# Kernel optimization log

Hardware: AMD Instinct MI355X
Metric: run time of the kernel (lower is better)

## Reference

```python
import jax, jax.numpy as jnp
from jax import lax
import numpy as np

D_MODEL = 1024
D_STATE = 16
D_CONV = 4
EXPAND = 2
D_INNER = EXPAND * D_MODEL  # 2048
DT_RANK = D_MODEL // 16     # 64
BATCH = 2
SEQLEN = 1024


def setup_inputs() -> dict:
    key = jax.random.key(0)
    ks = iter(jax.random.split(key, 32))

    def nrm(shape, s=0.02):
        return jax.random.normal(next(ks), shape, jnp.float32) * s

    def mamba_params():
        return dict(
            Win=nrm((2 * D_INNER, D_MODEL)), bin=jnp.zeros((2 * D_INNER,), jnp.float32),
            convw=nrm((D_INNER, D_CONV), 0.1), convb=jnp.zeros((D_INNER,), jnp.float32),
            Wx=nrm((DT_RANK + 2 * D_STATE, D_INNER)),
            Wdt=nrm((D_INNER, DT_RANK), 0.1), bdt=nrm((D_INNER,), 0.1),
            Alog=jnp.log(jnp.broadcast_to(jnp.arange(1, D_STATE + 1, dtype=jnp.float32), (D_INNER, D_STATE))),
            Dsk=jnp.ones((D_INNER,), jnp.float32),
            Wout=nrm((D_MODEL, D_INNER)), bout=jnp.zeros((D_MODEL,), jnp.float32),
        )

    inp = {"x": jax.random.normal(next(ks), (BATCH, SEQLEN, D_MODEL), jnp.float32)}
    for pref, p in (("f_", mamba_params()), ("b_", mamba_params())):
        for k, v in p.items():
            inp[pref + k] = v
    inp["proj_W"] = nrm((D_MODEL, 2 * D_MODEL))
    inp["proj_b"] = jnp.zeros((D_MODEL,), jnp.float32)
    return inp


def selective_scan(u, delta, A, Bm, Cm, Dsk):
    # u, delta: (B,L,Di); Bm, Cm: (B,L,N); A: (Di,N); Dsk: (Di,)
    def step(h, inp):
        u_t, d_t, b_t, c_t = inp  # (B,Di),(B,Di),(B,N),(B,N)
        dA = jnp.exp(d_t[..., None] * A)                      # (B,Di,N)
        h = h * dA + (d_t * u_t)[..., None] * b_t[:, None, :]  # (B,Di,N)
        y = jnp.einsum('bdn,bn->bd', h, c_t)
        return h, y

    h0 = jnp.zeros((u.shape[0], A.shape[0], A.shape[1]), u.dtype)
    xs = (u.transpose(1, 0, 2), delta.transpose(1, 0, 2),
          Bm.transpose(1, 0, 2), Cm.transpose(1, 0, 2))
    _, ys = lax.scan(step, h0, xs)
    return ys.transpose(1, 0, 2) + u * Dsk  # (B,L,Di)


def mamba_fwd(x, Win, bin_, convw, convb, Wx, Wdt, bdt, Alog, Dsk, Wout, bout):
    xz = x @ Win.T + bin_                      # (B,L,2*Di)
    xin, z = jnp.split(xz, 2, axis=-1)
    # causal depthwise conv over time: (B,Di,L)
    xc = lax.conv_general_dilated(
        xin.transpose(0, 2, 1), convw[:, None, :], (1,), [(D_CONV - 1, 0)],
        dimension_numbers=('NCH', 'OIH', 'NCH'), feature_group_count=D_INNER)
    u = jax.nn.silu(xc.transpose(0, 2, 1) + convb)  # (B,L,Di)
    xdbl = u @ Wx.T                                 # (B,L,dt_rank+2N)
    dt, Bm, Cm = jnp.split(xdbl, [DT_RANK, DT_RANK + D_STATE], axis=-1)
    delta = jax.nn.softplus(dt @ Wdt.T + bdt)       # (B,L,Di)
    A = -jnp.exp(Alog)
    y = selective_scan(u, delta, A, Bm, Cm, Dsk)
    y = y * jax.nn.silu(z)
    return y @ Wout.T + bout


def reference(x,
              f_Win, f_bin, f_convw, f_convb, f_Wx, f_Wdt, f_bdt, f_Alog, f_Dsk, f_Wout, f_bout,
              b_Win, b_bin, b_convw, b_convb, b_Wx, b_Wdt, b_bdt, b_Alog, b_Dsk, b_Wout, b_bout,
              proj_W, proj_b):
    out_f = mamba_fwd(x, f_Win, f_bin, f_convw, f_convb, f_Wx, f_Wdt, f_bdt, f_Alog, f_Dsk, f_Wout, f_bout)
    xr = jnp.flip(x, axis=1)
    out_b = mamba_fwd(xr, b_Win, b_bin, b_convw, b_convb, b_Wx, b_Wdt, b_bdt, b_Alog, b_Dsk, b_Wout, b_bout)
    out_b = jnp.flip(out_b, axis=1)
    out = jnp.concatenate([out_f, out_b], axis=-1)  # (B,L,2*d_model)
    return out @ proj_W.T + proj_b
```

## Files before the change

### kernel.cpp

```cpp
#include <hip/hip_runtime.h>
#include <math.h>

#define D_MODEL 1024
#define D_STATE 16
#define D_CONV  4
#define D_INNER 2048
#define DT_RANK 64
#define BATCH   2
#define SEQLEN  1024
#define MROWS   2048
#define XDBL_LD 128
#define NCHUNK  32
#define CLEN    (SEQLEN / NCHUNK)
#define NCHG    8192

typedef __attribute__((ext_vector_type(8))) short bf16x8;
typedef __attribute__((ext_vector_type(4))) float f32x4;

#define BARR() asm volatile("s_barrier" ::: "memory")
#define VMW(n) asm volatile("s_waitcnt vmcnt(" #n ")" ::: "memory")
#define LGKM(n) asm volatile("s_waitcnt lgkmcnt(" #n ")" ::: "memory")
#define SCHB() __builtin_amdgcn_sched_barrier(0)

static __device__ __forceinline__ float sigmoidf_(float x) {
    return 1.f / (1.f + __expf(-x));
}
static __device__ __forceinline__ unsigned short bf16rn(float f) {
    unsigned u = __float_as_uint(f);
    return (unsigned short)((u + 0x7FFFu + ((u >> 16) & 1u)) >> 16);
}
static __device__ __forceinline__ void hl_split(float f, unsigned short& h, unsigned short& l) {
    h = bf16rn(f);
    l = bf16rn(f - __uint_as_float((unsigned)h << 16));
}
static __device__ __forceinline__ float us2f(unsigned short u) {
    return __uint_as_float((unsigned)u << 16);
}

static __device__ __forceinline__
void split_block(const float* __restrict__ in, int R, int C, int ldin,
                 unsigned short* __restrict__ out, int Rout, bool flip,
                 int blk, int tid)
{
    int q = blk * 256 + tid;
    int qpr = C >> 2;
    int row = q / qpr;
    int c4 = (q - row * qpr) << 2;
    if (row >= Rout) return;
    unsigned short h[4] = {0, 0, 0, 0}, l[4] = {0, 0, 0, 0};
    if (row < R) {
        int sr = row;
        if (flip) { int b = row >> 10, t = row & 1023; sr = (b << 10) + (1023 - t); }
        float4 v = *(const float4*)(in + (size_t)sr * ldin + c4);
        float f[4] = {v.x, v.y, v.z, v.w};
        #pragma unroll
        for (int i = 0; i < 4; ++i) hl_split(f[i], h[i], l[i]);
    }
    size_t ob = (size_t)row * (2 * C);
    *(ushort4*)(out + ob + c4)     = make_ushort4(h[0], h[1], h[2], h[3]);
    *(ushort4*)(out + ob + C + c4) = make_ushort4(l[0], l[1], l[2], l[3]);
}

__global__ __launch_bounds__(256)
void prep1_kernel(const float* __restrict__ x,
                  const float* __restrict__ Win0, const float* __restrict__ Win1,
                  const float* __restrict__ Wx0,  const float* __restrict__ Wx1,
                  const float* __restrict__ Wdt0, const float* __restrict__ Wdt1,
                  unsigned short* xc0,
                  unsigned short* Winb0, unsigned short* Winb1,
                  unsigned short* Wxb0, unsigned short* Wxb1,
                  unsigned short* Wdtb0, unsigned short* Wdtb1)
{
    int b = blockIdx.x, tid = threadIdx.x;
    if      (b < 2048)  split_block(x,    MROWS, D_MODEL, D_MODEL, xc0,  MROWS, false, b,        tid);
    else if (b < 6144)  split_block(Win0, 4096,  D_MODEL, D_MODEL, Winb0, 4096, false, b - 2048, tid);
    else if (b < 10240) split_block(Win1, 4096,  D_MODEL, D_MODEL, Winb1, 4096, false, b - 6144, tid);
    else if (b < 10496) split_block(Wx0,  96,    D_INNER, D_INNER, Wxb0,  128,  false, b - 10240, tid);
    else if (b < 10752) split_block(Wx1,  96,    D_INNER, D_INNER, Wxb1,  128,  false, b - 10496, tid);
    else if (b < 10880) split_block(Wdt0, D_INNER, DT_RANK, DT_RANK, Wdtb0, D_INNER, false, b - 10752, tid);
    else                split_block(Wdt1, D_INNER, DT_RANK, DT_RANK, Wdtb1, D_INNER, false, b - 10880, tid);
}

#define SWZ(row) (((row) >> 1) & 3)
#define RDA(p, kk, row) (*(const bf16x8*)&AS[p][kk][row][(fs ^ SWZ(row)) << 3])
#define RDB(p, kk, row) (*(const bf16x8*)&BS[p][kk][row][(fs ^ SWZ(row)) << 3])

#define MFMA16(ACCBASE, AF, BF) \
    _Pragma("unroll") for (int f = 0; f < 4; ++f) \
    _Pragma("unroll") for (int g = 0; g < 4; ++g) \
        acc[(ACCBASE) + f][g] = __builtin_amdgcn_mfma_f32_16x16x32_bf16(AF[f], BF[g], acc[(ACCBASE) + f][g], 0, 0, 0);

#define KTILE(MODE, kt) do { \
    const int p_ = (kt) & 1; \
    const int pn_ = ((kt) + 1) & 1; \
    {  \
        if (MODE < 2) stageA((kt) + 1, 1); \
        BARR(); \
        _Pragma("unroll") for (int f = 0; f < 4; ++f) { int rw = wm + 64 + f * 16 + fr; aFB[f] = RDA(p_, 0, rw); } \
        LGKM(4); SCHB(); \
        __builtin_amdgcn_s_setprio(1); \
        MFMA16(0, aFA, bFA) \
        __builtin_amdgcn_s_setprio(0); \
    } \
    {  \
        if (MODE == 0) stageB((kt) + 2, 0); \
        BARR(); \
        _Pragma("unroll") for (int f = 0; f < 4; ++f) { int rw = wm + f * 16 + fr; aFA[f] = RDA(p_, 1, rw); } \
        _Pragma("unroll") for (int g = 0; g < 4; ++g) { int rw = wn + g * 16 + fr; bFB[g] = RDB(p_, 1, rw); } \
        LGKM(8); SCHB(); \
        __builtin_amdgcn_s_setprio(1); \
        MFMA16(4, aFB, bFA) \
        __builtin_amdgcn_s_setprio(0); \
    } \
    {  \
        if (MODE == 0) stageA((kt) + 2, 0); \
        BARR(); \
        _Pragma("unroll") for (int f = 0; f < 4; ++f) { int rw = wm + 64 + f * 16 + fr; aFB[f] = RDA(p_, 1, rw); } \
        LGKM(4); SCHB(); \
        __builtin_amdgcn_s_setprio(1); \
        MFMA16(0, aFA, bFB) \
        __builtin_amdgcn_s_setprio(0); \
    } \
    {  \
        if (MODE == 0) { VMW(4); } else if (MODE == 1) { VMW(0); } \
        if (MODE == 0) stageB((kt) + 2, 1); \
        BARR(); \
        if (MODE < 2) { \
            _Pragma("unroll") for (int f = 0; f < 4; ++f) { int rw = wm + f * 16 + fr; aFA[f] = RDA(pn_, 0, rw); } \
            _Pragma("unroll") for (int g = 0; g < 4; ++g) { int rw = wn + g * 16 + fr; bFA[g] = RDB(pn_, 0, rw); } \
            LGKM(8); \
        } else { LGKM(0); } \
        SCHB(); \
        __builtin_amdgcn_s_setprio(1); \
        MFMA16(4, aFB, bFB) \
        __builtin_amdgcn_s_setprio(0); \
    } \
} while (0)

template<int ACT, bool PART, int KTS, bool DUALN>
__global__ __launch_bounds__(512, 1)
void gemm256(const unsigned short* __restrict__ A0,
             const unsigned short* __restrict__ A1,
             const unsigned short* __restrict__ W0,
             const unsigned short* __restrict__ W1,
             const float* __restrict__ bias0,
             const float* __restrict__ bias1,
             float* __restrict__ C0, float* __restrict__ C1,
             float* __restrict__ part,
             int ldc, int N, int K, int nks)
{
    __shared__ unsigned short AS[2][2][256][32];
    __shared__ unsigned short BS[2][2][256][32];

    const int tid = threadIdx.x;
    const int lane = tid & 63;
    const int wid = tid >> 6;

    const int z = blockIdx.z;
    const int zdir = z / nks;
    const int ks = z - zdir * nks;

    const int nbx = gridDim.x;
    const int nwg = nbx * gridDim.y;
    int bid = blockIdx.y * nbx + blockIdx.x;
    int q8 = nwg >> 3;
    int swz = (bid & 7) * q8 + (bid >> 3);
    const int bm = (swz / nbx) * 256;
    const int bn = (swz % nbx) * 256;

    int dn, bnn;
    if (DUALN) { dn = (bn >= (N >> 1)) ? 1 : 0; bnn = bn - dn * (N >> 1); }
    else       { dn = zdir; bnn = bn; }
    const unsigned short* A = (DUALN || dn == 0) ? A0 : A1;
    const unsigned short* W = dn ? W1 : W0;

    const int ldg = 2 * K;
    constexpr int NT = 3 * KTS;
    const int Kc = KTS * 64;
    const int kbase = ks * Kc;

    const int wm = (wid >> 2) * 128;
    const int wn = (wid & 3) * 64;
    const int fr = lane & 15;
    const int fs = lane >> 4;

    f32x4 acc[8][4];
    #pragma unroll
    for (int i = 0; i < 8; ++i)
        #pragma unroll
        for (int j = 0; j < 4; ++j) {
            f32x4 zv = {0.f, 0.f, 0.f, 0.f};
            acc[i][j] = zv;
        }

    auto koffA = [&](int t) { unsigned tu = (unsigned)t; unsigned sg = tu / KTS;
                              unsigned w = tu - sg * KTS;
                              return (int)((sg == 1 ? (unsigned)K : 0u) + kbase + w * 64); };
    auto koffB = [&](int t) { unsigned tu = (unsigned)t; unsigned sg = tu / KTS;
                              unsigned w = tu - sg * KTS;
                              return (int)((sg == 2 ? (unsigned)K : 0u) + kbase + w * 64); };

    auto stageA = [&](int t, int kk) {
        int ko = koffA(t) + kk * 32;
        unsigned short* dst = &AS[t & 1][kk][0][0];
        #pragma unroll
        for (int i = 0; i < 2; ++i) {
            int s = i * 512 + tid;
            int row = s >> 2, sl = s & 3, lsl = sl ^ SWZ(row);
            const unsigned short* src = A + (size_t)(bm + row) * ldg + ko + lsl * 8;
            __builtin_amdgcn_global_load_lds(
                (const __attribute__((address_space(1))) void*)src,
                (__attribute__((address_space(3))) void*)(dst + s * 8), 16, 0, 0);
        }
    };
    auto stageB = [&](int t, int kk) {
        int ko = koffB(t) + kk * 32;
        unsigned short* dst = &BS[t & 1][kk][0][0];
        #pragma unroll
        for (int i = 0; i < 2; ++i) {
            int s = i * 512 + tid;
            int row = s >> 2, sl = s & 3, lsl = sl ^ SWZ(row);
            const unsigned short* src = W + (size_t)(bnn + row) * ldg + ko + lsl * 8;
            __builtin_amdgcn_global_load_lds(
                (const __attribute__((address_space(1))) void*)src,
                (__attribute__((address_space(3))) void*)(dst + s * 8), 16, 0, 0);
        }
    };

    stageB(0, 0); stageA(0, 0); stageB(0, 1); stageA(0, 1);
    stageB(1, 0); stageA(1, 0); stageB(1, 1);
    VMW(6);
    BARR();

    bf16x8 aFA[4], aFB[4], bFA[4], bFB[4];
    #pragma unroll
    for (int f = 0; f < 4; ++f) { int rw = wm + f * 16 + fr; aFA[f] = RDA(0, 0, rw); }
    #pragma unroll
    for (int g = 0; g < 4; ++g) { int rw = wn + g * 16 + fr; bFA[g] = RDB(0, 0, rw); }

    #pragma unroll 1
    for (int kt = 0; kt < NT - 2; ++kt) KTILE(0, kt);
    KTILE(1, NT - 2);
    KTILE(2, NT - 1);

    if (PART) {
        float* P = part + (size_t)z * ((size_t)MROWS * N);
        #pragma unroll
        for (int i = 0; i < 8; ++i)
            #pragma unroll
            for (int j = 0; j < 4; ++j) {
                int coln = bnn + wn + j * 16 + fr;
                #pragma unroll
                for (int r = 0; r < 4; ++r) {
                    int rowm = bm + wm + i * 16 + fs * 4 + r;
                    P[(size_t)rowm * N + coln] = acc[i][j][r];
                }
            }
    } else {
        const float* bias = dn ? bias1 : bias0;
        float* C = dn ? C1 : C0;
        #pragma unroll
        for (int i = 0; i < 8; ++i)
            #pragma unroll
            for (int j = 0; j < 4; ++j) {
                int coln = bnn + wn + j * 16 + fr;
                float bv = bias ? bias[coln] : 0.f;
                #pragma unroll
                for (int r = 0; r < 4; ++r) {
                    int rowm = bm + wm + i * 16 + fs * 4 + r;
                    float v = acc[i][j][r] + bv;
                    if (ACT == 1) v = (v > 20.f) ? v : log1pf(__expf(v));
                    int crow = rowm;
                    if (DUALN && dn) { int bb = rowm >> 10, t = rowm & 1023; crow = (bb << 10) + 1023 - t; }
                    C[(size_t)crow * ldc + coln] = v;
                }
            }
    }
}

template<int ACT, bool PART>
__global__ __launch_bounds__(256)
void gemm_mfma(const unsigned short* __restrict__ A0,
               const unsigned short* __restrict__ A1,
               const unsigned short* __restrict__ W0,
               const unsigned short* __restrict__ W1,
               const float* __restrict__ bias0,
               const float* __restrict__ bias1,
               float* __restrict__ C0, float* __restrict__ C1,
               float* __restrict__ part,
               int ldc, int N, int K, int nks)
{
    __shared__ __align__(16) unsigned short As[128 * 32];
    __shared__ __align__(16) unsigned short Bs[128 * 32];

    const int tid = threadIdx.x;
    const int lane = tid & 63;
    const int wid = tid >> 6;

    const int z = blockIdx.z;
    const int dir = z / nks;
    const int ks = z - dir * nks;
    const unsigned short* A = dir ? A1 : A0;
    const unsigned short* W = dir ? W1 : W0;

    const int nbx = gridDim.x;
    const int nwg = nbx * gridDim.y;
    int bid = blockIdx.y * nbx + blockIdx.x;
    int q8 = nwg >> 3;
    int swz = (nwg >= 8) ? (bid & 7) * q8 + (bid >> 3) : bid;
    const int bm = (swz / nbx) * 128;
    const int bn = (swz % nbx) * 128;

    const int ldg = 2 * K;
    const int Kc = K / nks;
    const int kbase = ks * Kc;

    f32x4 acc[4][4];
    #pragma unroll
    for (int i = 0; i < 4; ++i)
        #pragma unroll
        for (int j = 0; j < 4; ++j) {
            f32x4 zv = {0.f, 0.f, 0.f, 0.f};
            acc[i][j] = zv;
        }

    const int r0 = tid >> 2;
    const int k0s = (tid & 3) ^ ((r0 >> 1) & 3);
    const int r1 = (256 + tid) >> 2;
    const int k1s = (tid & 3) ^ ((r1 >> 1) & 3);

    unsigned short* As_w0 = &As[(tid >> 2) * 32 + ((tid & 3) << 3)];
    unsigned short* As_w1 = As_w0 + 64 * 32;
    unsigned short* Bs_w0 = &Bs[(tid >> 2) * 32 + ((tid & 3) << 3)];
    unsigned short* Bs_w1 = Bs_w0 + 64 * 32;

    const int wm = (wid >> 1) * 64;
    const int wn = (wid & 1) * 64;
    const int fr = lane & 15;
    const int fs = lane >> 4;

    const int KS = Kc >> 5;
    #pragma unroll 1
    for (int seg = 0; seg < 3; ++seg) {
        const int aoff = ((seg == 1) ? K : 0) + kbase;
        const int boff = ((seg == 2) ? K : 0) + kbase;
        #pragma unroll 1
        for (int kt = 0; kt < KS; ++kt) {
            const int kk = kt << 5;
            const unsigned short* ga0 = A + (size_t)(bm + r0) * ldg + aoff + kk + k0s * 8;
            const unsigned short* ga1 = A + (size_t)(bm + r1) * ldg + aoff + kk + k1s * 8;
            const unsigned short* gw0 = W + (size_t)(bn + r0) * ldg + boff + kk + k0s * 8;
            const unsigned short* gw1 = W + (size_t)(bn + r1) * ldg + boff + kk + k1s * 8;
            __builtin_amdgcn_global_load_lds(
                (const __attribute__((address_space(1))) void*)ga0,
                (__attribute__((address_space(3))) void*)As_w0, 16, 0, 0);
            __builtin_amdgcn_global_load_lds(
                (const __attribute__((address_space(1))) void*)ga1,
                (__attribute__((address_space(3))) void*)As_w1, 16, 0, 0);
            __builtin_amdgcn_global_load_lds(
                (const __attribute__((address_space(1))) void*)gw0,
                (__attribute__((address_space(3))) void*)Bs_w0, 16, 0, 0);
            __builtin_amdgcn_global_load_lds(
                (const __attribute__((address_space(1))) void*)gw1,
                (__attribute__((address_space(3))) void*)Bs_w1, 16, 0, 0);
            __syncthreads();

            bf16x8 aF[4], bF[4];
            #pragma unroll
            for (int f = 0; f < 4; ++f) {
                int ra = wm + f * 16 + fr;
                int sa = fs ^ ((ra >> 1) & 3);
                aF[f] = *(const bf16x8*)&As[ra * 32 + sa * 8];
                int rb = wn + f * 16 + fr;
                int sb = fs ^ ((rb >> 1) & 3);
                bF[f] = *(const bf16x8*)&Bs[rb * 32 + sb * 8];
            }
            #pragma unroll
            for (int i = 0; i < 4; ++i)
                #pragma unroll
                for (int j = 0; j < 4; ++j)
                    acc[i][j] = __builtin_amdgcn_mfma_f32_16x16x32_bf16(
                        aF[i], bF[j], acc[i][j], 0, 0, 0);
            __syncthreads();
        }
    }

    if (PART) {
        float* P = part + (size_t)z * ((size_t)MROWS * N);
        #pragma unroll
        for (int i = 0; i < 4; ++i)
            #pragma unroll
            for (int j = 0; j < 4; ++j) {
                int coln = bn + wn + j * 16 + fr;
                #pragma unroll
                for (int r = 0; r < 4; ++r) {
                    int rowm = bm + wm + i * 16 + fs * 4 + r;
                    P[(size_t)rowm * N + coln] = acc[i][j][r];
                }
            }
    } else {
        const float* bias = dir ? bias1 : bias0;
        float* C = dir ? C1 : C0;
        #pragma unroll
        for (int i = 0; i < 4; ++i)
            #pragma unroll
            for (int j = 0; j < 4; ++j) {
                int coln = bn + wn + j * 16 + fr;
                float bv = bias ? bias[coln] : 0.f;
                #pragma unroll
                for (int r = 0; r < 4; ++r) {
                    int rowm = bm + wm + i * 16 + fs * 4 + r;
                    float v = acc[i][j][r] + bv;
                    if (ACT == 1) v = (v > 20.f) ? v : log1pf(__expf(v));
                    C[(size_t)rowm * ldc + coln] = v;
                }
            }
    }
}

__global__ __launch_bounds__(256)
void reduce_xdbl_k(const float* __restrict__ part,
                   float* __restrict__ xdbl0, float* __restrict__ xdbl1,
                   unsigned short* __restrict__ dtb0, unsigned short* __restrict__ dtb1)
{
    const int dz = blockIdx.z;
    const float* P = part + (size_t)dz * 16 * MROWS * XDBL_LD;
    float* xdbl = dz ? xdbl1 : xdbl0;
    unsigned short* dtb = dz ? dtb1 : dtb0;
    int i = blockIdx.x * 256 + threadIdx.x;
    int row = i >> 5;
    int c4 = (i & 31) << 2;
    float4 s = make_float4(0.f, 0.f, 0.f, 0.f);
    #pragma unroll
    for (int k = 0; k < 16; ++k) {
        float4 v = *(const float4*)(P + (size_t)k * MROWS * XDBL_LD + (size_t)row * XDBL_LD + c4);
        s.x += v.x; s.y += v.y; s.z += v.z; s.w += v.w;
    }
    *(float4*)(xdbl + (size_t)row * XDBL_LD + c4) = s;
    if (c4 < DT_RANK) {
        float f[4] = {s.x, s.y, s.z, s.w};
        unsigned short h[4], l[4];
        #pragma unroll
        for (int j = 0; j < 4; ++j) hl_split(f[j], h[j], l[j]);
        *(ushort4*)(dtb + (size_t)row * (2 * DT_RANK) + c4) = make_ushort4(h[0], h[1], h[2], h[3]);
        *(ushort4*)(dtb + (size_t)row * (2 * DT_RANK) + DT_RANK + c4) = make_ushort4(l[0], l[1], l[2], l[3]);
    }
}

__global__ __launch_bounds__(256)
void mid_kernel(const float* __restrict__ part2,
                const float* __restrict__ bout0, const float* __restrict__ bout1,
                unsigned short* __restrict__ tmpb,
                const float* __restrict__ projW, unsigned short* __restrict__ pWb)
{
    const int dz = blockIdx.z;
    const int tid = threadIdx.x;
    if (dz == 2) {
        split_block(projW, D_MODEL, 2 * D_MODEL, 2 * D_MODEL, pWb, D_MODEL, false, blockIdx.x, tid);
        return;
    }
    const float* P = part2 + (size_t)dz * 4 * MROWS * D_MODEL;
    const float* bias = dz ? bout1 : bout0;
    const int colofs = dz ? D_MODEL : 0;
    int i = blockIdx.x * 256 + tid;
    int row = i >> 8;
    int c4 = (i & 255) << 2;
    float4 s = make_float4(bias[c4], bias[c4 + 1], bias[c4 + 2], bias[c4 + 3]);
    #pragma unroll
    for (int k = 0; k < 4; ++k) {
        float4 v = *(const float4*)(P + (size_t)k * MROWS * D_MODEL + (size_t)row * D_MODEL + c4);
        s.x += v.x; s.y += v.y; s.z += v.z; s.w += v.w;
    }
    int orow = row;
    if (dz) { int bb = row >> 10, t = row & 1023; orow = (bb << 10) + 1023 - t; }
    float f[4] = {s.x, s.y, s.z, s.w};
    unsigned short h[4], l[4];
    #pragma unroll
    for (int j = 0; j < 4; ++j) hl_split(f[j], h[j], l[j]);
    *(ushort4*)(tmpb + (size_t)orow * 4096 + colofs + c4) = make_ushort4(h[0], h[1], h[2], h[3]);
    *(ushort4*)(tmpb + (size_t)orow * 4096 + 2048 + colofs + c4) = make_ushort4(l[0], l[1], l[2], l[3]);
}

__global__ __launch_bounds__(256)
void reduce_out_k(const float* __restrict__ part, const float* __restrict__ bias,
                  float* __restrict__ out)
{
    int i = blockIdx.x * 256 + threadIdx.x;
    int row = i >> 8;
    int c4 = (i & 255) << 2;
    float4 s = make_float4(bias[c4], bias[c4 + 1], bias[c4 + 2], bias[c4 + 3]);
    #pragma unroll
    for (int k = 0; k < 8; ++k) {
        float4 v = *(const float4*)(part + (size_t)k * MROWS * D_MODEL + (size_t)row * D_MODEL + c4);
        s.x += v.x; s.y += v.y; s.z += v.z; s.w += v.w;
    }
    *(float4*)(out + (size_t)row * D_MODEL + c4) = s;
}

__global__ __launch_bounds__(256)
void conv_prep_kernel(const float* __restrict__ xz0, const float* __restrict__ xz1,
                      const float* __restrict__ cw0, const float* __restrict__ cw1,
                      const float* __restrict__ cb0, const float* __restrict__ cb1,
                      unsigned short* __restrict__ ub0, unsigned short* __restrict__ ub1,
                      const float* __restrict__ Wout0, const float* __restrict__ Wout1,
                      unsigned short* __restrict__ Woutb0, unsigned short* __restrict__ Woutb1)
{
    const int dz = blockIdx.z;
    const int tid = threadIdx.x;
    if (dz == 2) {
        int b = blockIdx.x;
        if (b < 2048) split_block(Wout0, D_MODEL, D_INNER, D_INNER, Woutb0, D_MODEL, false, b, tid);
        else if (b < 4096) split_block(Wout1, D_MODEL, D_INNER, D_INNER, Woutb1, D_MODEL, false, b - 2048, tid);
        return;
    }
    const float* xz = dz ? xz1 : xz0;
    const float* convw = dz ? cw1 : cw0;
    const float* convb = dz ? cb1 : cb0;
    unsigned short* ub = dz ? ub1 : ub0;
    int idx = blockIdx.x * 256 + tid;
    int d = idx % D_INNER;
    int r = idx / D_INNER;
    int t = r % SEQLEN;
    float acc = convb[d];
    #pragma unroll
    for (int k = 0; k < D_CONV; ++k) {
        int back = D_CONV - 1 - k;
        if (t - back >= 0)
            acc += xz[(size_t)(r - back) * (2 * D_INNER) + d] * convw[d * D_CONV + k];
    }
    float v = acc * sigmoidf_(acc);
    unsigned short h, l;
    hl_split(v, h, l);
    ub[(size_t)r * (2 * D_INNER) + d] = h;
    ub[(size_t)r * (2 * D_INNER) + D_INNER + d] = l;
}

__global__ __launch_bounds__(256)
void scan_phase1(const float* __restrict__ delta0, const float* __restrict__ delta1,
                 const unsigned short* __restrict__ ub0, const unsigned short* __restrict__ ub1,
                 const float* __restrict__ xdbl0, const float* __restrict__ xdbl1,
                 const float* __restrict__ Alog0, const float* __restrict__ Alog1,
                 float* __restrict__ aprod, float* __restrict__ hfin)
{
    const int gid = blockIdx.x * 256 + threadIdx.x;
    const int chg = gid & (NCHG - 1);
    const int chunk = gid >> 13;
    const int dir = chg >> 12;
    const int bd = chg & 4095;
    const int b = bd >> 11, d = bd & 2047;
    const float* delta = dir ? delta1 : delta0;
    const unsigned short* ub = dir ? ub1 : ub0;
    const float* xdbl = dir ? xdbl1 : xdbl0;
    const float* Alog = dir ? Alog1 : Alog0;

    float Av[16], h[16], ap[16];
    #pragma unroll
    for (int n = 0; n < 16; ++n) {
        Av[n] = -__expf(Alog[d * D_STATE + n]);
        h[n] = 0.f; ap[n] = 1.f;
    }
    const int t0 = chunk * CLEN;
    for (int t = t0; t < t0 + CLEN; ++t) {
        const size_t r = (size_t)b * SEQLEN + t;
        float dlt = delta[r * D_INNER + d];
        float uu = us2f(ub[r * 4096 + d]) + us2f(ub[r * 4096 + 2048 + d]);
        float du = dlt * uu;
        float4 bq[4];
        #pragma unroll
        for (int q = 0; q < 4; ++q)
            bq[q] = *(const float4*)(xdbl + r * XDBL_LD + DT_RANK + q * 4);
        #pragma unroll
        for (int n = 0; n < 16; ++n) {
            float Bv = ((const float*)&bq[n >> 2])[n & 3];
            float dA = __expf(dlt * Av[n]);
            h[n] = h[n] * dA + du * Bv;
            ap[n] *= dA;
        }
    }
    float* pa = aprod + (size_t)chunk * (NCHG * 16) + (size_t)chg * 16;
    float* pf = hfin  + (size_t)chunk * (NCHG * 16) + (size_t)chg * 16;
    #pragma unroll
    for (int q = 0; q < 4; ++q) {
        *(float4*)(pa + q * 4) = make_float4(ap[q*4], ap[q*4+1], ap[q*4+2], ap[q*4+3]);
        *(float4*)(pf + q * 4) = make_float4(h[q*4], h[q*4+1], h[q*4+2], h[q*4+3]);
    }
}

__global__ __launch_bounds__(256)
void scan_phase2(float* __restrict__ aprod ,
                 const float* __restrict__ hfin)
{
    const int gid = blockIdx.x * 256 + threadIdx.x;
    float h = 0.f;
    for (int c = 0; c < NCHUNK; ++c) {
        const size_t idx = (size_t)c * (NCHG * 16) + gid;
        float a = aprod[idx];
        float f = hfin[idx];
        aprod[idx] = h;
        h = a * h + f;
    }
}

__global__ __launch_bounds__(256)
void scan_phase3(const float* __restrict__ delta0, const float* __restrict__ delta1,
                 unsigned short* __restrict__ ub0, unsigned short* __restrict__ ub1,
                 const float* __restrict__ xdbl0, const float* __restrict__ xdbl1,
                 const float* __restrict__ Alog0, const float* __restrict__ Alog1,
                 const float* __restrict__ Dsk0, const float* __restrict__ Dsk1,
                 const float* __restrict__ xz0, const float* __restrict__ xz1,
                 const float* __restrict__ hin)
{
    const int gid = blockIdx.x * 256 + threadIdx.x;
    const int chg = gid & (NCHG - 1);
    const int chunk = gid >> 13;
    const int dir = chg >> 12;
    const int bd = chg & 4095;
    const int b = bd >> 11, d = bd & 2047;
    const float* delta = dir ? delta1 : delta0;
    unsigned short* ub = dir ? ub1 : ub0;
    const float* xdbl = dir ? xdbl1 : xdbl0;
    const float* Alog = dir ? Alog1 : Alog0;
    const float* Dsk = dir ? Dsk1 : Dsk0;
    const float* xz = dir ? xz1 : xz0;

    float Av[16], h[16];
    const float* ph = hin + (size_t)chunk * (NCHG * 16) + (size_t)chg * 16;
    #pragma unroll
    for (int n = 0; n < 16; ++n) {
        Av[n] = -__expf(Alog[d * D_STATE + n]);
        h[n] = ph[n];
    }
    const float Dv = Dsk[d];
    const int t0 = chunk * CLEN;
    for (int t = t0; t < t0 + CLEN; ++t) {
        const size_t r = (size_t)b * SEQLEN + t;
        float dlt = delta[r * D_INNER + d];
        float uu = us2f(ub[r * 4096 + d]) + us2f(ub[r * 4096 + 2048 + d]);
        float du = dlt * uu;
        float4 bq[4], cq[4];
        #pragma unroll
        for (int q = 0; q < 4; ++q) {
            bq[q] = *(const float4*)(xdbl + r * XDBL_LD + DT_RANK + q * 4);
            cq[q] = *(const float4*)(xdbl + r * XDBL_LD + DT_RANK + D_STATE + q * 4);
        }
        float p0 = 0.f, p1 = 0.f, p2 = 0.f, p3 = 0.f;
        #pragma unroll
        for (int n = 0; n < 16; ++n) {
            float Bv = ((const float*)&bq[n >> 2])[n & 3];
            float Cv = ((const float*)&cq[n >> 2])[n & 3];
            float dA = __expf(dlt * Av[n]);
            h[n] = h[n] * dA + du * Bv;
            if ((n & 3) == 0) p0 += h[n] * Cv;
            else if ((n & 3) == 1) p1 += h[n] * Cv;
            else if ((n & 3) == 2) p2 += h[n] * Cv;
            else p3 += h[n] * Cv;
        }
        float y = ((p0 + p1) + (p2 + p3)) + uu * Dv;
        float zv = xz[r * (2 * D_INNER) + D_INNER + d];
        float v = y * (zv * sigmoidf_(zv));
        unsigned short hh, ll;
        hl_split(v, hh, ll);
        ub[r * 4096 + d] = hh;
        ub[r * 4096 + 2048 + d] = ll;
    }
}

extern "C" void kernel_launch(void* const* d_in, const int* in_sizes, int n_in,
                              void* d_out, int out_size, void* d_ws, size_t ws_size,
                              hipStream_t stream)
{
    const float* x = (const float*)d_in[0];
    const float* proj_W = (const float*)d_in[23];
    const float* proj_b = (const float*)d_in[24];
    float* out = (float*)d_out;

    const float *Win[2], *bin_[2], *convw[2], *convb[2], *Wx[2], *Wdt[2], *bdt[2],
                *Alog[2], *Dsk[2], *Wout[2], *bout[2];
    for (int dir = 0; dir < 2; ++dir) {
        const int base = 1 + dir * 11;
        Win[dir]   = (const float*)d_in[base + 0];
        bin_[dir]  = (const float*)d_in[base + 1];
        convw[dir] = (const float*)d_in[base + 2];
        convb[dir] = (const float*)d_in[base + 3];
        Wx[dir]    = (const float*)d_in[base + 4];
        Wdt[dir]   = (const float*)d_in[base + 5];
        bdt[dir]   = (const float*)d_in[base + 6];
        Alog[dir]  = (const float*)d_in[base + 7];
        Dsk[dir]   = (const float*)d_in[base + 8];
        Wout[dir]  = (const float*)d_in[base + 9];
        bout[dir]  = (const float*)d_in[base + 10];
    }

    char* ws = (char*)d_ws;
    const size_t MB = 1ull << 20;
    float* xz[2]            = {(float*)(ws + 0 * MB),   (float*)(ws + 32 * MB)};
    unsigned short* ub[2]   = {(unsigned short*)(ws + 64 * MB),
                               (unsigned short*)(ws + 80 * MB)};
    unsigned short* Winb[2] = {(unsigned short*)(ws + 96 * MB),
                               (unsigned short*)(ws + 112 * MB)};
    unsigned short* xc0     = (unsigned short*)(ws + 128 * MB);
    float* part             = (float*)(ws + 112 * MB);
    float* part2            = (float*)(ws + 0 * MB);
    float* delta[2]         = {(float*)(ws + 112 * MB), (float*)(ws + 128 * MB)};
    unsigned short* Woutb[2]= {(unsigned short*)(ws + 96 * MB),
                               (unsigned short*)(ws + 104 * MB)};
    unsigned short* yzb[2]  = {ub[0], ub[1]};
    unsigned short* tmpb    = ub[0];
    unsigned short* pWb     = ub[1];
    unsigned short* Wxb[2]  = {(unsigned short*)(ws + 144 * MB), (unsigned short*)(ws + 145 * MB)};
    unsigned short* Wdtb[2] = {(unsigned short*)(ws + 146 * MB), (unsigned short*)(ws + 146 * MB + 512 * 1024)};
    unsigned short* dtb[2]  = {(unsigned short*)(ws + 147 * MB), (unsigned short*)(ws + 147 * MB + 512 * 1024)};
    float* xdbl[2]          = {(float*)(ws + 148 * MB), (float*)(ws + 149 * MB)};
    float* aprod            = (float*)(ws + 150 * MB);
    float* hfin             = (float*)(ws + 167 * MB);

    dim3 blk(256);

    prep1_kernel<<<11008, blk, 0, stream>>>(
        x, Win[0], Win[1], Wx[0], Wx[1], Wdt[0], Wdt[1],
        xc0, Winb[0], Winb[1], Wxb[0], Wxb[1], Wdtb[0], Wdtb[1]);

    gemm256<0, false, 16, true><<<dim3(32, 8, 1), dim3(512), 0, stream>>>(
        xc0, nullptr, Winb[0], Winb[1], bin_[0], bin_[1], xz[0], xz[1],
        nullptr, 4096, 8192, D_MODEL, 1);

    conv_prep_kernel<<<dim3((MROWS * D_INNER) / 256, 1, 3), blk, 0, stream>>>(
        xz[0], xz[1], convw[0], convw[1], convb[0], convb[1], ub[0], ub[1],
        Wout[0], Wout[1], Woutb[0], Woutb[1]);

    gemm_mfma<0, true><<<dim3(1, 16, 32), blk, 0, stream>>>(
        ub[0], ub[1], Wxb[0], Wxb[1], nullptr, nullptr, nullptr, nullptr,
        part, XDBL_LD, XDBL_LD, D_INNER, 16);

    reduce_xdbl_k<<<dim3(256, 1, 2), blk, 0, stream>>>(
        part, xdbl[0], xdbl[1], dtb[0], dtb[1]);

    gemm_mfma<1, false><<<dim3(16, 16, 2), blk, 0, stream>>>(
        dtb[0], dtb[1], Wdtb[0], Wdtb[1], bdt[0], bdt[1], delta[0], delta[1],
        nullptr, D_INNER, D_INNER, DT_RANK, 1);

    scan_phase1<<<NCHUNK * NCHG / 256, blk, 0, stream>>>(
        delta[0], delta[1], ub[0], ub[1], xdbl[0], xdbl[1], Alog[0], Alog[1],
        aprod, hfin);
    scan_phase2<<<NCHG * 16 / 256, blk, 0, stream>>>(aprod, hfin);
    scan_phase3<<<NCHUNK * NCHG / 256, blk, 0, stream>>>(
        delta[0], delta[1], ub[0], ub[1], xdbl[0], xdbl[1], Alog[0], Alog[1],
        Dsk[0], Dsk[1], xz[0], xz[1], aprod);

    gemm256<0, true, 8, false><<<dim3(4, 8, 8), dim3(512), 0, stream>>>(
        yzb[0], yzb[1], Woutb[0], Woutb[1], nullptr, nullptr, nullptr, nullptr,
        part2, D_MODEL, D_MODEL, D_INNER, 4);

    mid_kernel<<<dim3(2048, 1, 3), blk, 0, stream>>>(
        part2, bout[0], bout[1], tmpb, proj_W, pWb);

    gemm256<0, true, 4, false><<<dim3(4, 8, 8), dim3(512), 0, stream>>>(
        tmpb, nullptr, pWb, nullptr, nullptr, nullptr, nullptr, nullptr,
        part2, D_MODEL, D_MODEL, 2 * D_MODEL, 8);

    reduce_out_k<<<2048, blk, 0, stream>>>(part2, proj_b, out);
}
```

Baseline: 459.0 us.

## Replace 256x256 GEMM tiles with 128x128 tiles and halve split-K partitions

The 512-thread 256x256-tile GEMM is replaced by a 256-thread 128x128-tile kernel with two blocks per CU, a simpler double-buffered k-loop and half the accumulators. Split-K factors for the output and projection GEMMs are halved, and the reduction kernels are updated to match, which cuts partial-sum traffic. More and smaller blocks should improve occupancy and load balance across CUs. The cost is less data reuse per tile, so more global and LDS traffic is needed per FLOP.

```diff
diff --git a/kernel.cpp b/kernel.cpp
--- a/kernel.cpp
+++ b/kernel.cpp
@@ -85,72 +85,53 @@
 #define RDA(p, kk, row) (*(const bf16x8*)&AS[p][kk][row][(fs ^ SWZ(row)) << 3])
 #define RDB(p, kk, row) (*(const bf16x8*)&BS[p][kk][row][(fs ^ SWZ(row)) << 3])
 
-#define MFMA16(ACCBASE, AF, BF) \
+#define MFMA16(AF, BF) \
     _Pragma("unroll") for (int f = 0; f < 4; ++f) \
     _Pragma("unroll") for (int g = 0; g < 4; ++g) \
-        acc[(ACCBASE) + f][g] = __builtin_amdgcn_mfma_f32_16x16x32_bf16(AF[f], BF[g], acc[(ACCBASE) + f][g], 0, 0, 0);
-
-#define KTILE(MODE, kt) do { \
+        acc[f][g] = __builtin_amdgcn_mfma_f32_16x16x32_bf16(AF[f], BF[g], acc[f][g], 0, 0, 0);
+
+#define KT128(MODE, kt) do { \
     const int p_ = (kt) & 1; \
     const int pn_ = ((kt) + 1) & 1; \
     {  \
-        if (MODE < 2) stageA((kt) + 1, 1); \
+        if (MODE == 0) { stageA((kt) + 1, 0); stageB((kt) + 1, 0); VMW(4); } \
+        else { VMW(0); } \
         BARR(); \
-        _Pragma("unroll") for (int f = 0; f < 4; ++f) { int rw = wm + 64 + f * 16 + fr; aFB[f] = RDA(p_, 0, rw); } \
-        LGKM(4); SCHB(); \
+        _Pragma("unroll") for (int f = 0; f < 4; ++f) { int rw = wm + f * 16 + fr; aFB[f] = RDA(p_, 1, rw); } \
+        _Pragma("unroll") for (int g = 0; g < 4; ++g) { int rw = wn + g * 16 + fr; bFB[g] = RDB(p_, 1, rw); } \
+        LGKM(8); SCHB(); \
         __builtin_amdgcn_s_setprio(1); \
-        MFMA16(0, aFA, bFA) \
+        MFMA16(aFA, bFA) \
         __builtin_amdgcn_s_setprio(0); \
     } \
     {  \
-        if (MODE == 0) stageB((kt) + 2, 0); \
-        BARR(); \
-        _Pragma("unroll") for (int f = 0; f < 4; ++f) { int rw = wm + f * 16 + fr; aFA[f] = RDA(p_, 1, rw); } \
-        _Pragma("unroll") for (int g = 0; g < 4; ++g) { int rw = wn + g * 16 + fr; bFB[g] = RDB(p_, 1, rw); } \
-        LGKM(8); SCHB(); \
-        __builtin_amdgcn_s_setprio(1); \
-        MFMA16(4, aFB, bFA) \
-        __builtin_amdgcn_s_setprio(0); \
-    } \
-    {  \
-        if (MODE == 0) stageA((kt) + 2, 0); \
-        BARR(); \
-        _Pragma("unroll") for (int f = 0; f < 4; ++f) { int rw = wm + 64 + f * 16 + fr; aFB[f] = RDA(p_, 1, rw); } \
-        LGKM(4); SCHB(); \
-        __builtin_amdgcn_s_setprio(1); \
-        MFMA16(0, aFA, bFB) \
-        __builtin_amdgcn_s_setprio(0); \
-    } \
-    {  \
-        if (MODE == 0) { VMW(4); } else if (MODE == 1) { VMW(0); } \
-        if (MODE == 0) stageB((kt) + 2, 1); \
-        BARR(); \
-        if (MODE < 2) { \
+        if (MODE == 0) { \
+            stageA((kt) + 1, 1); stageB((kt) + 1, 1); VMW(4); BARR(); \
             _Pragma("unroll") for (int f = 0; f < 4; ++f) { int rw = wm + f * 16 + fr; aFA[f] = RDA(pn_, 0, rw); } \
             _Pragma("unroll") for (int g = 0; g < 4; ++g) { int rw = wn + g * 16 + fr; bFA[g] = RDB(pn_, 0, rw); } \
             LGKM(8); \
         } else { LGKM(0); } \
         SCHB(); \
         __builtin_amdgcn_s_setprio(1); \
-        MFMA16(4, aFB, bFB) \
+        MFMA16(aFB, bFB) \
         __builtin_amdgcn_s_setprio(0); \
     } \
 } while (0)
 
 template<int ACT, bool PART, int KTS, bool DUALN>
-__global__ __launch_bounds__(512, 1)
-void gemm256(const unsigned short* __restrict__ A0,
-             const unsigned short* __restrict__ A1,
-             const unsigned short* __restrict__ W0,
-             const unsigned short* __restrict__ W1,
-             const float* __restrict__ bias0,
-             const float* __restrict__ bias1,
-             float* __restrict__ C0, float* __restrict__ C1,
-             float* __restrict__ part,
-             int ldc, int N, int K, int nks)
-{
-    __shared__ unsigned short AS[2][2][256][32];
-    __shared__ unsigned short BS[2][2][256][32];
+__global__ __launch_bounds__(256, 2)
+void gemm128p(const unsigned short* __restrict__ A0,
+              const unsigned short* __restrict__ A1,
+              const unsigned short* __restrict__ W0,
+              const unsigned short* __restrict__ W1,
+              const float* __restrict__ bias0,
+              const float* __restrict__ bias1,
+              float* __restrict__ C0, float* __restrict__ C1,
+              float* __restrict__ part,
+              int ldc, int N, int K, int nks)
+{
+    __shared__ unsigned short AS[2][2][128][32];
+    __shared__ unsigned short BS[2][2][128][32];
 
     const int tid = threadIdx.x;
     const int lane = tid & 63;
@@ -165,8 +146,8 @@
     int bid = blockIdx.y * nbx + blockIdx.x;
     int q8 = nwg >> 3;
     int swz = (bid & 7) * q8 + (bid >> 3);
-    const int bm = (swz / nbx) * 256;
-    const int bn = (swz % nbx) * 256;
+    const int bm = (swz / nbx) * 128;
+    const int bn = (swz % nbx) * 128;
 
     int dn, bnn;
     if (DUALN) { dn = (bn >= (N >> 1)) ? 1 : 0; bnn = bn - dn * (N >> 1); }
@@ -179,14 +160,14 @@
     const int Kc = KTS * 64;
     const int kbase = ks * Kc;
 
-    const int wm = (wid >> 2) * 128;
-    const int wn = (wid & 3) * 64;
+    const int wm = (wid >> 1) * 64;
+    const int wn = (wid & 1) * 64;
     const int fr = lane & 15;
     const int fs = lane >> 4;
 
-    f32x4 acc[8][4];
-    #pragma unroll
-    for (int i = 0; i < 8; ++i)
+    f32x4 acc[4][4];
+    #pragma unroll
+    for (int i = 0; i < 4; ++i)
         #pragma unroll
         for (int j = 0; j < 4; ++j) {
             f32x4 zv = {0.f, 0.f, 0.f, 0.f};
@@ -205,7 +186,7 @@
         unsigned short* dst = &AS[t & 1][kk][0][0];
         #pragma unroll
         for (int i = 0; i < 2; ++i) {
-            int s = i * 512 + tid;
+            int s = i * 256 + tid;
             int row = s >> 2, sl = s & 3, lsl = sl ^ SWZ(row);
             const unsigned short* src = A + (size_t)(bm + row) * ldg + ko + lsl * 8;
             __builtin_amdgcn_global_load_lds(
@@ -218,7 +199,7 @@
         unsigned short* dst = &BS[t & 1][kk][0][0];
         #pragma unroll
         for (int i = 0; i < 2; ++i) {
-            int s = i * 512 + tid;
+            int s = i * 256 + tid;
             int row = s >> 2, sl = s & 3, lsl = sl ^ SWZ(row);
             const unsigned short* src = W + (size_t)(bnn + row) * ldg + ko + lsl * 8;
             __builtin_amdgcn_global_load_lds(
@@ -227,9 +208,8 @@
         }
     };
 
-    stageB(0, 0); stageA(0, 0); stageB(0, 1); stageA(0, 1);
-    stageB(1, 0); stageA(1, 0); stageB(1, 1);
-    VMW(6);
+    stageA(0, 0); stageB(0, 0); stageA(0, 1); stageB(0, 1);
+    VMW(4);
     BARR();
 
     bf16x8 aFA[4], aFB[4], bFA[4], bFB[4];
@@ -239,14 +219,13 @@
     for (int g = 0; g < 4; ++g) { int rw = wn + g * 16 + fr; bFA[g] = RDB(0, 0, rw); }
 
     #pragma unroll 1
-    for (int kt = 0; kt < NT - 2; ++kt) KTILE(0, kt);
-    KTILE(1, NT - 2);
-    KTILE(2, NT - 1);
+    for (int kt = 0; kt < NT - 1; ++kt) KT128(0, kt);
+    KT128(2, NT - 1);
 
     if (PART) {
         float* P = part + (size_t)z * ((size_t)MROWS * N);
         #pragma unroll
-        for (int i = 0; i < 8; ++i)
+        for (int i = 0; i < 4; ++i)
             #pragma unroll
             for (int j = 0; j < 4; ++j) {
                 int coln = bnn + wn + j * 16 + fr;
@@ -260,7 +239,7 @@
         const float* bias = dn ? bias1 : bias0;
         float* C = dn ? C1 : C0;
         #pragma unroll
-        for (int i = 0; i < 8; ++i)
+        for (int i = 0; i < 4; ++i)
             #pragma unroll
             for (int j = 0; j < 4; ++j) {
                 int coln = bnn + wn + j * 16 + fr;
@@ -459,7 +438,7 @@
         split_block(projW, D_MODEL, 2 * D_MODEL, 2 * D_MODEL, pWb, D_MODEL, false, blockIdx.x, tid);
         return;
     }
-    const float* P = part2 + (size_t)dz * 4 * MROWS * D_MODEL;
+    const float* P = part2 + (size_t)dz * 2 * MROWS * D_MODEL;
     const float* bias = dz ? bout1 : bout0;
     const int colofs = dz ? D_MODEL : 0;
     int i = blockIdx.x * 256 + tid;
@@ -467,7 +446,7 @@
     int c4 = (i & 255) << 2;
     float4 s = make_float4(bias[c4], bias[c4 + 1], bias[c4 + 2], bias[c4 + 3]);
     #pragma unroll
-    for (int k = 0; k < 4; ++k) {
+    for (int k = 0; k < 2; ++k) {
         float4 v = *(const float4*)(P + (size_t)k * MROWS * D_MODEL + (size_t)row * D_MODEL + c4);
         s.x += v.x; s.y += v.y; s.z += v.z; s.w += v.w;
     }
@@ -490,7 +469,7 @@
     int c4 = (i & 255) << 2;
     float4 s = make_float4(bias[c4], bias[c4 + 1], bias[c4 + 2], bias[c4 + 3]);
     #pragma unroll
-    for (int k = 0; k < 8; ++k) {
+    for (int k = 0; k < 4; ++k) {
         float4 v = *(const float4*)(part + (size_t)k * MROWS * D_MODEL + (size_t)row * D_MODEL + c4);
         s.x += v.x; s.y += v.y; s.z += v.z; s.w += v.w;
     }
@@ -720,7 +699,7 @@
         x, Win[0], Win[1], Wx[0], Wx[1], Wdt[0], Wdt[1],
         xc0, Winb[0], Winb[1], Wxb[0], Wxb[1], Wdtb[0], Wdtb[1]);
 
-    gemm256<0, false, 16, true><<<dim3(32, 8, 1), dim3(512), 0, stream>>>(
+    gemm128p<0, false, 16, true><<<dim3(64, 16, 1), blk, 0, stream>>>(
         xc0, nullptr, Winb[0], Winb[1], bin_[0], bin_[1], xz[0], xz[1],
         nullptr, 4096, 8192, D_MODEL, 1);
 
@@ -747,16 +726,16 @@
         delta[0], delta[1], ub[0], ub[1], xdbl[0], xdbl[1], Alog[0], Alog[1],
         Dsk[0], Dsk[1], xz[0], xz[1], aprod);
 
-    gemm256<0, true, 8, false><<<dim3(4, 8, 8), dim3(512), 0, stream>>>(
+    gemm128p<0, true, 16, false><<<dim3(8, 16, 4), blk, 0, stream>>>(
         yzb[0], yzb[1], Woutb[0], Woutb[1], nullptr, nullptr, nullptr, nullptr,
-        part2, D_MODEL, D_MODEL, D_INNER, 4);
+        part2, D_MODEL, D_MODEL, D_INNER, 2);
 
     mid_kernel<<<dim3(2048, 1, 3), blk, 0, stream>>>(
         part2, bout[0], bout[1], tmpb, proj_W, pWb);
 
-    gemm256<0, true, 4, false><<<dim3(4, 8, 8), dim3(512), 0, stream>>>(
+    gemm128p<0, true, 8, false><<<dim3(8, 16, 4), blk, 0, stream>>>(
         tmpb, nullptr, pWb, nullptr, nullptr, nullptr, nullptr, nullptr,
-        part2, D_MODEL, D_MODEL, 2 * D_MODEL, 8);
+        part2, D_MODEL, D_MODEL, 2 * D_MODEL, 4);
 
     reduce_out_k<<<2048, blk, 0, stream>>>(part2, proj_b, out);
 }
```

After: 496.6 us. 8.2% more time.
